# Optimization experiments

Measured on AMD Instinct MI355X. Metric: run time of the kernel, lower is better.

The kernel has to match this reference:

```python
import jax, jax.numpy as jnp
import numpy as np

B, S, D_IN = 4, 2048, 1024
N_HEAD, D_ATTN, D_OUT = 16, 64, 1024
D_H = N_HEAD * D_ATTN  # 1024; NOTE: no head split in original module


def setup_inputs() -> dict:
    key = jax.random.key(0)
    ks = jax.random.split(key, 12)
    s = 1.0 / np.sqrt(D_IN)
    inp = {
        "q": jax.random.normal(ks[0], (B, S, D_IN), dtype=jnp.float32),
        "k": jax.random.normal(ks[1], (B, S, D_IN), dtype=jnp.float32),
        "v": jax.random.normal(ks[2], (B, S, D_IN), dtype=jnp.float32),
        "mask": jax.random.randint(ks[3], (B, S, S), 0, 2, dtype=jnp.int32),
        "Wq": jax.random.normal(ks[4], (D_H, D_IN), dtype=jnp.float32) * s,
        "bq": jnp.zeros((D_H,), dtype=jnp.float32),
        "Wk": jax.random.normal(ks[5], (D_H, D_IN), dtype=jnp.float32) * s,
        "bk": jnp.zeros((D_H,), dtype=jnp.float32),
        "Wv": jax.random.normal(ks[6], (D_H, D_IN), dtype=jnp.float32) * s,
        "bv": jnp.zeros((D_H,), dtype=jnp.float32),
        "Wo": jax.random.normal(ks[7], (D_OUT, D_H), dtype=jnp.float32) * (1.0 / np.sqrt(D_H)),
        "bo": jnp.zeros((D_OUT,), dtype=jnp.float32),
    }
    return inp


def reference(q, k, v, mask, Wq, bq, Wk, bk, Wv, bv, Wo, bo):
    # manual QKV projections (torch Linear: x @ W.T + b)
    Q = q @ Wq.T + bq  # [B,S,D_H]
    K = k @ Wk.T + bk
    V = v @ Wv.T + bv
    d_k = Q.shape[-1]  # full concatenated dim (no head split, faithful)
    e = jnp.einsum("bsd,btd->bst", Q, K) / jnp.sqrt(jnp.float32(d_k))  # [B,S,S]
    MASK_FILL = jnp.float32(-(2 ** 15))  # original uses -2**15 regardless of dtype
    e = jnp.where(mask == 0, MASK_FILL, e)
    a = jax.nn.softmax(e, axis=-1)
    y = jnp.einsum("bst,btd->bsd", a, V)  # [B,S,D_H]
    return y @ Wo.T + bo  # [B,S,D_OUT]
```

## Files before the change

### kernel.cpp

```cpp
#include <hip/hip_runtime.h>
#include <hip/hip_bf16.h>

#define B_   4
#define S_   2048
#define DIN  1024
#define DH   1024
#define DOUT 1024

typedef __attribute__((ext_vector_type(8))) __bf16 bf16x8;
typedef __attribute__((ext_vector_type(4))) float floatx4;
typedef unsigned short u16;
typedef unsigned int u32;

__device__ inline u16 f2bf(float f) {
  union { float f; u32 u; } x; x.f = f;
  u32 r = x.u + 0x7fffu + ((x.u >> 16) & 1u);
  return (u16)(r >> 16);
}

__global__ __launch_bounds__(256)
void cast_f32_bf16(const float* __restrict__ in, u16* __restrict__ out, long n4) {
  long i = (long)blockIdx.x * 256 + threadIdx.x;
  if (i >= n4) return;
  float4 v = ((const float4*)in)[i];
  ushort4 o;
  o.x = f2bf(v.x); o.y = f2bf(v.y); o.z = f2bf(v.z); o.w = f2bf(v.w);
  ((ushort4*)out)[i] = o;
}

__global__ __launch_bounds__(256)
void gather_bias(const float* __restrict__ b0, const float* __restrict__ b1,
                 const float* __restrict__ b2, float* __restrict__ dst) {
  int i = blockIdx.x * 256 + threadIdx.x;
  if (i < DH) dst[i] = b0[i];
  else if (i < 2 * DH) dst[i] = b1[i - DH];
  else if (i < 3 * DH) dst[i] = b2[i - 2 * DH];
}

__global__ __launch_bounds__(256)
void transpose_bf16(const u16* __restrict__ in, u16* __restrict__ out) {
  __shared__ u16 t[32][33];
  const int b = blockIdx.z;
  const int r0 = blockIdx.y * 32, c0 = blockIdx.x * 32;
  const int tx = threadIdx.x & 31, ty = threadIdx.x >> 5;
  const u16* ib = in + (long)b * S_ * DH;
  u16* ob = out + (long)b * DH * S_;
#pragma unroll
  for (int i = 0; i < 4; ++i) {
    int r = ty + i * 8;
    t[r][tx] = ib[(long)(r0 + r) * DH + (c0 + tx)];
  }
  __syncthreads();
#pragma unroll
  for (int i = 0; i < 4; ++i) {
    int r = ty + i * 8;
    ob[(long)(c0 + r) * S_ + (r0 + tx)] = t[tx][r];
  }
}

__global__ __launch_bounds__(256)
void softmax_row(const u16* __restrict__ E, u16* __restrict__ A) {
  const long row = blockIdx.x;
  const _Float16* e = (const _Float16*)(E + row * (long)S_);
  u16* a = A + row * (long)S_;
  const int tid = threadIdx.x;
  const int w = tid >> 6, l = tid & 63;
  __shared__ float sred[8];

  typedef __attribute__((ext_vector_type(8))) _Float16 f16x8;
  f16x8 ev = *(const f16x8*)(e + tid * 8);
  float p[8];
#pragma unroll
  for (int j = 0; j < 8; ++j) p[j] = (float)ev[j];

  float mx = p[0];
#pragma unroll
  for (int j = 1; j < 8; ++j) mx = fmaxf(mx, p[j]);
#pragma unroll
  for (int o = 32; o > 0; o >>= 1) mx = fmaxf(mx, __shfl_xor(mx, o));
  if (l == 0) sred[w] = mx;
  __syncthreads();
  mx = fmaxf(fmaxf(sred[0], sred[1]), fmaxf(sred[2], sred[3]));

  float sum = 0.f;
#pragma unroll
  for (int j = 0; j < 8; ++j) { p[j] = __expf(p[j] - mx); sum += p[j]; }
#pragma unroll
  for (int o = 32; o > 0; o >>= 1) sum += __shfl_xor(sum, o);
  if (l == 0) sred[4 + w] = sum;
  __syncthreads();
  sum = sred[4] + sred[5] + sred[6] + sred[7];
  const float inv = 1.0f / sum;

  ushort4 o0, o1;
  o0.x = f2bf(p[0] * inv); o0.y = f2bf(p[1] * inv);
  o0.z = f2bf(p[2] * inv); o0.w = f2bf(p[3] * inv);
  o1.x = f2bf(p[4] * inv); o1.y = f2bf(p[5] * inv);
  o1.z = f2bf(p[6] * inv); o1.w = f2bf(p[7] * inv);
  ((ushort4*)a)[tid * 2]     = o0;
  ((ushort4*)a)[tid * 2 + 1] = o1;
}

#define EPI_BF16_BIAS 0
#define EPI_F16_MASK  1
#define EPI_BF16      2
#define EPI_F32_BIAS  3

#define BARRIER() do { asm volatile("" ::: "memory"); __builtin_amdgcn_s_barrier(); \
                       asm volatile("" ::: "memory"); } while (0)
#define WAITVM(N) asm volatile("s_waitcnt vmcnt(" #N ")" ::: "memory")

template <int EPI, int BN>
__global__ __launch_bounds__(512, 2)
void gemm256(const u16* __restrict__ A, const u16* __restrict__ Bm,
             void* __restrict__ C, const float* __restrict__ bias,
             const int* __restrict__ mask,
             int M, int N, int K, float scale,
             long sA, long sB, long sC, long sMask, long sBias,
             int nbx, int nby) {
  constexpr int NBR = BN / 128;
  constexpr int BUFSTRIDE = (2 + NBR) * 8192;
  constexpr int MFR = (BN == 256) ? 8 : 4;
  constexpr int MH  = MFR / 2;
  __shared__ u16 lds_[2 * BUFSTRIDE];

  const int tid = threadIdx.x;
  const int w  = tid >> 6;
  const int l  = tid & 63;
  const int wr = (BN == 256) ? (w >> 2) : (w >> 1);
  const int wc = (BN == 256) ? (w & 3) : (w & 1);
  const int lr = l & 15;
  const int q  = l >> 4;
  const int wrowb = wr * (MFR * 16);

  const int flat = blockIdx.x;
  const int cpx = (nbx * nby * gridDim.x / (nbx * nby)) >> 3;
  const int swz = (flat & 7) * (gridDim.x >> 3) + (flat >> 3);
  (void)cpx;
  const int bx = swz % nbx;
  const int rest = swz / nbx;
  const int by = rest % nby;
  const int bz = rest / nby;

  const long arow0 = (long)by * 256;
  const long bcol0 = (long)bx * BN;
  const u16* Ab = A + bz * sA + arow0 * K;
  const u16* Bb = Bm + bz * sB + bcol0 * K;

  const int nt = K >> 6;

  const int st_row = tid >> 3;
  const int st_ks  = (tid & 7) ^ (st_row & 7);

#define STAGE(GB, MATB, H, TT) do {                                           \
    const int _b = (TT) & 1;                                                  \
    const long _k0 = (long)(TT) * 64;                                         \
    _Pragma("unroll")                                                         \
    for (int _j = 0; _j < 2; ++_j) {                                          \
      const u16* _src = (GB) + (long)((H) * 128 + _j * 64 + st_row) * K       \
                        + _k0 + st_ks * 8;                                    \
      u16* _dst = &lds_[_b * BUFSTRIDE + ((MATB) + (H)) * 8192                \
                        + _j * 4096 + tid * 8];                               \
      __builtin_amdgcn_global_load_lds(                                       \
          (const __attribute__((address_space(1))) u32*)_src,                 \
          (__attribute__((address_space(3))) u32*)_dst, 16, 0, 0);            \
    }                                                                         \
  } while (0)

  floatx4 acc[MFR][4] = {};
  bf16x8 a[MH][2];
  bf16x8 b[2][2][2];

#define LDSOFF(BUF, MATB, _r, _s) \
    ((BUF) * BUFSTRIDE + ((MATB) + ((_r) >> 7)) * 8192 + ((_r) & 127) * 64 \
     + (((_s) ^ ((_r) & 7)) * 8))

#define LOAD_A(MHI, BUF) do {                                                 \
    _Pragma("unroll")                                                         \
    for (int _m = 0; _m < MH; ++_m)                                           \
      _Pragma("unroll")                                                       \
      for (int _kk = 0; _kk < 2; ++_kk) {                                     \
        const int _r = wrowb + (MHI) * (MH * 16) + _m * 16 + lr;              \
        const int _s = _kk * 4 + q;                                           \
        a[_m][_kk] = *(const bf16x8*)&lds_[LDSOFF(BUF, 0, _r, _s)];           \
      }                                                                       \
  } while (0)

#define LOAD_B(NHI, BUF) do {                                                 \
    _Pragma("unroll")                                                         \
    for (int _n = 0; _n < 2; ++_n)                                            \
      _Pragma("unroll")                                                       \
      for (int _kk = 0; _kk < 2; ++_kk) {                                     \
        const int _c = wc * 64 + (NHI) * 32 + _n * 16 + lr;                   \
        const int _s = _kk * 4 + q;                                           \
        b[NHI][_n][_kk] = *(const bf16x8*)&lds_[LDSOFF(BUF, 2, _c, _s)];      \
      }                                                                       \
  } while (0)

#define DO_Q(MHI, NHI) do {                                                   \
    __builtin_amdgcn_s_setprio(1);                                            \
    _Pragma("unroll")                                                         \
    for (int _m = 0; _m < MH; ++_m)                                           \
      _Pragma("unroll")                                                       \
      for (int _n = 0; _n < 2; ++_n)                                          \
        _Pragma("unroll")                                                     \
        for (int _kk = 0; _kk < 2; ++_kk)                                     \
          acc[(MHI)*MH + _m][(NHI)*2 + _n] = __builtin_amdgcn_mfma_f32_16x16x32_bf16( \
              a[_m][_kk], b[NHI][_n][_kk], acc[(MHI)*MH + _m][(NHI)*2 + _n], 0, 0, 0); \
    __builtin_amdgcn_s_setprio(0);                                            \
  } while (0)

  STAGE(Ab, 0, 0, 0); STAGE(Ab, 0, 1, 0);
  STAGE(Bb, 2, 0, 0); if constexpr (BN == 256) STAGE(Bb, 2, 1, 0);
  if (nt > 1) {
    STAGE(Bb, 2, 0, 1); if constexpr (BN == 256) STAGE(Bb, 2, 1, 1);
    if constexpr (BN == 256) { WAITVM(4); } else { WAITVM(2); }
  } else {
    WAITVM(0);
  }
  BARRIER();

  for (int t = 0; t < nt; ++t) {
    const int bmain = t & 1;
    LOAD_A(0, bmain); LOAD_B(0, bmain);
    if (t + 1 < nt) STAGE(Ab, 0, 0, t + 1);
    BARRIER();
    DO_Q(0, 0);
    BARRIER();
    LOAD_B(1, bmain);
    if (t + 1 < nt) STAGE(Ab, 0, 1, t + 1);
    BARRIER();
    DO_Q(0, 1);
    BARRIER();
    LOAD_A(1, bmain);
    if (t + 2 < nt) STAGE(Bb, 2, 0, t + 2);
    BARRIER();
    DO_Q(1, 1);
    BARRIER();
    if constexpr (BN == 256) { if (t + 2 < nt) STAGE(Bb, 2, 1, t + 2); }
    DO_Q(1, 0);
    if (t + 2 < nt) {
      if constexpr (BN == 256) { WAITVM(4); } else { WAITVM(2); }
    } else {
      WAITVM(0);
    }
    BARRIER();
  }

#undef STAGE
#undef LOAD_A
#undef LOAD_B
#undef DO_Q
#undef LDSOFF

  const int r4 = q * 4;
#pragma unroll
  for (int mf = 0; mf < MFR; ++mf)
#pragma unroll
    for (int nf = 0; nf < 4; ++nf)
#pragma unroll
      for (int r = 0; r < 4; ++r) {
        const long row = arow0 + wrowb + mf * 16 + r4 + r;
        const long col = bcol0 + wc * 64 + nf * 16 + lr;
        float v = acc[mf][nf][r];
        if constexpr (EPI == EPI_BF16_BIAS) {
          v += bias[bz * sBias + col];
          ((u16*)C)[bz * sC + row * N + col] = f2bf(v);
        } else if constexpr (EPI == EPI_BF16) {
          ((u16*)C)[bz * sC + row * N + col] = f2bf(v);
        } else if constexpr (EPI == EPI_F32_BIAS) {
          v += bias[bz * sBias + col];
          ((float*)C)[bz * sC + row * N + col] = v;
        } else {
          v *= scale;
          const int mk = mask[bz * sMask + row * (long)N + col];
          _Float16 hv = (_Float16)((mk == 0) ? -32768.0f : v);
          ((_Float16*)C)[bz * sC + row * N + col] = hv;
        }
      }
}

extern "C" void kernel_launch(void* const* d_in, const int* in_sizes, int n_in,
                              void* d_out, int out_size, void* d_ws, size_t ws_size,
                              hipStream_t stream) {
  const float* q    = (const float*)d_in[0];
  const float* k    = (const float*)d_in[1];
  const float* v    = (const float*)d_in[2];
  const int*   mask = (const int*)d_in[3];
  const float* Wq   = (const float*)d_in[4];
  const float* bq   = (const float*)d_in[5];
  const float* Wk   = (const float*)d_in[6];
  const float* bk   = (const float*)d_in[7];
  const float* Wv   = (const float*)d_in[8];
  const float* bv   = (const float*)d_in[9];
  const float* Wo   = (const float*)d_in[10];
  const float* bo   = (const float*)d_in[11];

  const long BS = (long)B_ * S_;
  const long nQ = BS * DH;
  const long nW = (long)DH * DIN;
  const long nE = (long)B_ * S_ * S_;

  char* ws = (char*)d_ws;
  size_t off = 0;
  auto alloc = [&](size_t bytes) {
    void* p = ws + off; off += (bytes + 255) & ~(size_t)255; return p;
  };

  u16* qb   = (u16*)alloc(nQ * 2);
  u16* kb   = (u16*)alloc(nQ * 2);
  u16* vb   = (u16*)alloc(nQ * 2);
  u16* wqb  = (u16*)alloc(nW * 2);
  u16* wkb  = (u16*)alloc(nW * 2);
  u16* wvb  = (u16*)alloc(nW * 2);
  u16* wob  = (u16*)alloc(nW * 2);
  u16* Qb   = (u16*)alloc(nQ * 2);
  u16* Kb   = (u16*)alloc(nQ * 2);
  u16* Vb   = (u16*)alloc(nQ * 2);
  u16* VT   = (u16*)alloc(nQ * 2);
  u16* E    = (u16*)alloc(nE * 2);
  float* bcat = (float*)alloc(3 * DH * 4);
  u16* Apb = qb;
  u16* Yb  = vb;

  auto cast = [&](const float* src, u16* dst, long n) {
    long n4 = n / 4;
    cast_f32_bf16<<<dim3((unsigned)((n4 + 255) / 256)), 256, 0, stream>>>(src, dst, n4);
  };
  cast(q, qb, nQ); cast(k, kb, nQ); cast(v, vb, nQ);
  cast(Wq, wqb, nW); cast(Wk, wkb, nW); cast(Wv, wvb, nW); cast(Wo, wob, nW);
  gather_bias<<<dim3(12), 256, 0, stream>>>(bq, bk, bv, bcat);

  gemm256<EPI_BF16_BIAS, 128><<<dim3(768), 512, 0, stream>>>(qb, wqb, Qb, bcat, nullptr,
      (int)BS, DH, DIN, 1.f, nQ, nW, nQ, 0, DH, DH / 128, (int)(BS / 256));

  {
    dim3 g(DH / 32, S_ / 32, B_);
    transpose_bf16<<<g, 256, 0, stream>>>(Vb, VT);
  }

  gemm256<EPI_F16_MASK, 256><<<dim3(256), 512, 0, stream>>>(Qb, Kb, (void*)E, nullptr, mask,
      S_, S_, DH, 0.03125f,
      (long)S_ * DH, (long)S_ * DH, (long)S_ * S_, (long)S_ * S_, 0,
      S_ / 256, S_ / 256);

  softmax_row<<<dim3((unsigned)(B_ * S_)), 256, 0, stream>>>(E, Apb);

  gemm256<EPI_BF16, 128><<<dim3(256), 512, 0, stream>>>(Apb, VT, Yb, nullptr, nullptr,
      S_, DH, S_, 1.f,
      (long)S_ * S_, (long)DH * S_, (long)S_ * DH, 0, 0,
      DH / 128, S_ / 256);

  gemm256<EPI_F32_BIAS, 128><<<dim3(256), 512, 0, stream>>>(Yb, wob, d_out, bo, nullptr,
      (int)BS, DOUT, DH, 1.f, 0, 0, 0, 0, 0,
      DOUT / 128, (int)(BS / 256));
}
```

Baseline: 247.9 us.

## Fuse softmax exp into QK GEMM epilogue and defer normalization to PV

```diff
diff --git a/kernel.cpp b/kernel.cpp
--- a/kernel.cpp
+++ b/kernel.cpp
@@ -18,14 +18,31 @@
   return (u16)(r >> 16);
 }
 
+#define BARRIER() do { asm volatile("" ::: "memory"); __builtin_amdgcn_s_barrier(); \
+                       asm volatile("" ::: "memory"); } while (0)
+#define WAITVM(N) asm volatile("s_waitcnt vmcnt(" #N ")" ::: "memory")
+
 __global__ __launch_bounds__(256)
-void cast_f32_bf16(const float* __restrict__ in, u16* __restrict__ out, long n4) {
-  long i = (long)blockIdx.x * 256 + threadIdx.x;
-  if (i >= n4) return;
-  float4 v = ((const float4*)in)[i];
+void cast_all(const float* __restrict__ q, const float* __restrict__ k,
+              const float* __restrict__ v, const float* __restrict__ w0,
+              const float* __restrict__ w1, const float* __restrict__ w2,
+              const float* __restrict__ w3, u16* __restrict__ dst) {
+  const long nQ = (long)B_ * S_ * DIN;
+  const long nW = (long)DH * DIN;
+  long b = blockIdx.x;
+  const float* src; long doff;
+  if (b < 8192)       { src = q;  doff = 0;            }
+  else if (b < 16384) { src = k;  doff = nQ;     b -= 8192;  }
+  else if (b < 24576) { src = v;  doff = 2 * nQ; b -= 16384; }
+  else if (b < 25600) { src = w0; doff = 3 * nQ; b -= 24576; }
+  else if (b < 26624) { src = w1; doff = 3 * nQ + nW;     b -= 25600; }
+  else if (b < 27648) { src = w2; doff = 3 * nQ + 2 * nW; b -= 26624; }
+  else                { src = w3; doff = 3 * nQ + 3 * nW; b -= 27648; }
+  long i = b * 256 + threadIdx.x;
+  float4 vv = ((const float4*)src)[i];
   ushort4 o;
-  o.x = f2bf(v.x); o.y = f2bf(v.y); o.z = f2bf(v.z); o.w = f2bf(v.w);
-  ((ushort4*)out)[i] = o;
+  o.x = f2bf(vv.x); o.y = f2bf(vv.y); o.z = f2bf(vv.z); o.w = f2bf(vv.w);
+  ((ushort4*)(dst + doff))[i] = o;
 }
 
 __global__ __launch_bounds__(256)
@@ -59,100 +76,47 @@
 }
 
 __global__ __launch_bounds__(256)
-void softmax_row(const u16* __restrict__ E, u16* __restrict__ A) {
-  const long row = blockIdx.x;
-  const _Float16* e = (const _Float16*)(E + row * (long)S_);
-  u16* a = A + row * (long)S_;
-  const int tid = threadIdx.x;
-  const int w = tid >> 6, l = tid & 63;
-  __shared__ float sred[8];
-
-  typedef __attribute__((ext_vector_type(8))) _Float16 f16x8;
-  f16x8 ev = *(const f16x8*)(e + tid * 8);
-  float p[8];
-#pragma unroll
-  for (int j = 0; j < 8; ++j) p[j] = (float)ev[j];
-
-  float mx = p[0];
-#pragma unroll
-  for (int j = 1; j < 8; ++j) mx = fmaxf(mx, p[j]);
-#pragma unroll
-  for (int o = 32; o > 0; o >>= 1) mx = fmaxf(mx, __shfl_xor(mx, o));
-  if (l == 0) sred[w] = mx;
-  __syncthreads();
-  mx = fmaxf(fmaxf(sred[0], sred[1]), fmaxf(sred[2], sred[3]));
-
-  float sum = 0.f;
-#pragma unroll
-  for (int j = 0; j < 8; ++j) { p[j] = __expf(p[j] - mx); sum += p[j]; }
-#pragma unroll
-  for (int o = 32; o > 0; o >>= 1) sum += __shfl_xor(sum, o);
-  if (l == 0) sred[4 + w] = sum;
-  __syncthreads();
-  sum = sred[4] + sred[5] + sred[6] + sred[7];
-  const float inv = 1.0f / sum;
-
-  ushort4 o0, o1;
-  o0.x = f2bf(p[0] * inv); o0.y = f2bf(p[1] * inv);
-  o0.z = f2bf(p[2] * inv); o0.w = f2bf(p[3] * inv);
-  o1.x = f2bf(p[4] * inv); o1.y = f2bf(p[5] * inv);
-  o1.z = f2bf(p[6] * inv); o1.w = f2bf(p[7] * inv);
-  ((ushort4*)a)[tid * 2]     = o0;
-  ((ushort4*)a)[tid * 2 + 1] = o1;
-}
-
-#define EPI_BF16_BIAS 0
-#define EPI_F16_MASK  1
-#define EPI_BF16      2
-#define EPI_F32_BIAS  3
-
-#define BARRIER() do { asm volatile("" ::: "memory"); __builtin_amdgcn_s_barrier(); \
-                       asm volatile("" ::: "memory"); } while (0)
-#define WAITVM(N) asm volatile("s_waitcnt vmcnt(" #N ")" ::: "memory")
-
-template <int EPI, int BN>
+void sumrows(const float* __restrict__ Psum, float* __restrict__ invs) {
+  int i = blockIdx.x * 256 + threadIdx.x;
+  const float4* p = (const float4*)(Psum + (long)i * 8);
+  float4 a = p[0], b = p[1];
+  float s = a.x + a.y + a.z + a.w + b.x + b.y + b.z + b.w;
+  invs[i] = 1.0f / s;
+}
+
 __global__ __launch_bounds__(512, 2)
-void gemm256(const u16* __restrict__ A, const u16* __restrict__ Bm,
-             void* __restrict__ C, const float* __restrict__ bias,
-             const int* __restrict__ mask,
-             int M, int N, int K, float scale,
-             long sA, long sB, long sC, long sMask, long sBias,
-             int nbx, int nby) {
-  constexpr int NBR = BN / 128;
-  constexpr int BUFSTRIDE = (2 + NBR) * 8192;
-  constexpr int MFR = (BN == 256) ? 8 : 4;
-  constexpr int MH  = MFR / 2;
+void gemm_pexp(const u16* __restrict__ Q, const u16* __restrict__ Kb_,
+               u16* __restrict__ P, const int* __restrict__ mask,
+               float* __restrict__ Psum) {
+  constexpr int BUFSTRIDE = 4 * 8192;
   __shared__ u16 lds_[2 * BUFSTRIDE];
 
   const int tid = threadIdx.x;
   const int w  = tid >> 6;
   const int l  = tid & 63;
-  const int wr = (BN == 256) ? (w >> 2) : (w >> 1);
-  const int wc = (BN == 256) ? (w & 3) : (w & 1);
+  const int wr = w >> 2;
+  const int wc = w & 3;
   const int lr = l & 15;
   const int q  = l >> 4;
-  const int wrowb = wr * (MFR * 16);
+  const int wrowb = wr * 128;
 
   const int flat = blockIdx.x;
-  const int cpx = (nbx * nby * gridDim.x / (nbx * nby)) >> 3;
-  const int swz = (flat & 7) * (gridDim.x >> 3) + (flat >> 3);
-  (void)cpx;
-  const int bx = swz % nbx;
-  const int rest = swz / nbx;
-  const int by = rest % nby;
-  const int bz = rest / nby;
+  const int swz = (flat & 7) * ((int)gridDim.x >> 3) + (flat >> 3);
+  const int bx = swz & 7;
+  const int by = (swz >> 3) & 7;
+  const int bz = swz >> 6;
 
   const long arow0 = (long)by * 256;
-  const long bcol0 = (long)bx * BN;
-  const u16* Ab = A + bz * sA + arow0 * K;
-  const u16* Bb = Bm + bz * sB + bcol0 * K;
-
+  const long bcol0 = (long)bx * 256;
+  const int K = DH;
+  const u16* Ab = Q + (long)bz * S_ * DH + arow0 * K;
+  const u16* Bb = Kb_ + (long)bz * S_ * DH + bcol0 * K;
   const int nt = K >> 6;
 
   const int st_row = tid >> 3;
   const int st_ks  = (tid & 7) ^ (st_row & 7);
 
-#define STAGE(GB, MATB, H, TT) do {                                           \
+#define PSTAGE(GB, MATB, H, TT) do {                                          \
     const int _b = (TT) & 1;                                                  \
     const long _k0 = (long)(TT) * 64;                                         \
     _Pragma("unroll")                                                         \
@@ -167,95 +131,260 @@
     }                                                                         \
   } while (0)
 
-  floatx4 acc[MFR][4] = {};
-  bf16x8 a[MH][2];
+  floatx4 acc[8][4] = {};
+  bf16x8 a[4][2];
   bf16x8 b[2][2][2];
 
-#define LDSOFF(BUF, MATB, _r, _s) \
+#define PLDSOFF(BUF, MATB, _r, _s) \
     ((BUF) * BUFSTRIDE + ((MATB) + ((_r) >> 7)) * 8192 + ((_r) & 127) * 64 \
      + (((_s) ^ ((_r) & 7)) * 8))
 
-#define LOAD_A(MHI, BUF) do {                                                 \
-    _Pragma("unroll")                                                         \
-    for (int _m = 0; _m < MH; ++_m)                                           \
+#define PLOAD_A(MHI, BUF) do {                                                \
+    _Pragma("unroll")                                                         \
+    for (int _m = 0; _m < 4; ++_m)                                            \
       _Pragma("unroll")                                                       \
       for (int _kk = 0; _kk < 2; ++_kk) {                                     \
-        const int _r = wrowb + (MHI) * (MH * 16) + _m * 16 + lr;              \
+        const int _r = wrowb + (MHI) * 64 + _m * 16 + lr;                     \
         const int _s = _kk * 4 + q;                                           \
-        a[_m][_kk] = *(const bf16x8*)&lds_[LDSOFF(BUF, 0, _r, _s)];           \
+        a[_m][_kk] = *(const bf16x8*)&lds_[PLDSOFF(BUF, 0, _r, _s)];          \
       }                                                                       \
   } while (0)
 
-#define LOAD_B(NHI, BUF) do {                                                 \
+#define PLOAD_B(NHI, BUF) do {                                                \
     _Pragma("unroll")                                                         \
     for (int _n = 0; _n < 2; ++_n)                                            \
       _Pragma("unroll")                                                       \
       for (int _kk = 0; _kk < 2; ++_kk) {                                     \
         const int _c = wc * 64 + (NHI) * 32 + _n * 16 + lr;                   \
         const int _s = _kk * 4 + q;                                           \
-        b[NHI][_n][_kk] = *(const bf16x8*)&lds_[LDSOFF(BUF, 2, _c, _s)];      \
+        b[NHI][_n][_kk] = *(const bf16x8*)&lds_[PLDSOFF(BUF, 2, _c, _s)];     \
       }                                                                       \
   } while (0)
 
-#define DO_Q(MHI, NHI) do {                                                   \
+#define PDO_Q(MHI, NHI) do {                                                  \
     __builtin_amdgcn_s_setprio(1);                                            \
     _Pragma("unroll")                                                         \
-    for (int _m = 0; _m < MH; ++_m)                                           \
+    for (int _m = 0; _m < 4; ++_m)                                            \
       _Pragma("unroll")                                                       \
       for (int _n = 0; _n < 2; ++_n)                                          \
         _Pragma("unroll")                                                     \
         for (int _kk = 0; _kk < 2; ++_kk)                                     \
-          acc[(MHI)*MH + _m][(NHI)*2 + _n] = __builtin_amdgcn_mfma_f32_16x16x32_bf16( \
-              a[_m][_kk], b[NHI][_n][_kk], acc[(MHI)*MH + _m][(NHI)*2 + _n], 0, 0, 0); \
+          acc[(MHI)*4 + _m][(NHI)*2 + _n] = __builtin_amdgcn_mfma_f32_16x16x32_bf16( \
+              a[_m][_kk], b[NHI][_n][_kk], acc[(MHI)*4 + _m][(NHI)*2 + _n], 0, 0, 0); \
     __builtin_amdgcn_s_setprio(0);                                            \
   } while (0)
 
-  STAGE(Ab, 0, 0, 0); STAGE(Ab, 0, 1, 0);
-  STAGE(Bb, 2, 0, 0); if constexpr (BN == 256) STAGE(Bb, 2, 1, 0);
-  if (nt > 1) {
-    STAGE(Bb, 2, 0, 1); if constexpr (BN == 256) STAGE(Bb, 2, 1, 1);
-    if constexpr (BN == 256) { WAITVM(4); } else { WAITVM(2); }
-  } else {
-    WAITVM(0);
-  }
+  PSTAGE(Ab, 0, 0, 0); PSTAGE(Ab, 0, 1, 0);
+  PSTAGE(Bb, 2, 0, 0); PSTAGE(Bb, 2, 1, 0);
+  PSTAGE(Bb, 2, 0, 1); PSTAGE(Bb, 2, 1, 1);
+  WAITVM(4);
   BARRIER();
 
   for (int t = 0; t < nt; ++t) {
     const int bmain = t & 1;
-    LOAD_A(0, bmain); LOAD_B(0, bmain);
-    if (t + 1 < nt) STAGE(Ab, 0, 0, t + 1);
-    BARRIER();
-    DO_Q(0, 0);
-    BARRIER();
-    LOAD_B(1, bmain);
-    if (t + 1 < nt) STAGE(Ab, 0, 1, t + 1);
-    BARRIER();
-    DO_Q(0, 1);
-    BARRIER();
-    LOAD_A(1, bmain);
-    if (t + 2 < nt) STAGE(Bb, 2, 0, t + 2);
-    BARRIER();
-    DO_Q(1, 1);
-    BARRIER();
-    if constexpr (BN == 256) { if (t + 2 < nt) STAGE(Bb, 2, 1, t + 2); }
-    DO_Q(1, 0);
-    if (t + 2 < nt) {
-      if constexpr (BN == 256) { WAITVM(4); } else { WAITVM(2); }
-    } else {
-      WAITVM(0);
+    PLOAD_A(0, bmain); PLOAD_B(0, bmain);
+    if (t + 1 < nt) PSTAGE(Ab, 0, 0, t + 1);
+    BARRIER();
+    PDO_Q(0, 0);
+    BARRIER();
+    PLOAD_B(1, bmain);
+    if (t + 1 < nt) PSTAGE(Ab, 0, 1, t + 1);
+    BARRIER();
+    PDO_Q(0, 1);
+    BARRIER();
+    PLOAD_A(1, bmain);
+    if (t + 2 < nt) PSTAGE(Bb, 2, 0, t + 2);
+    BARRIER();
+    PDO_Q(1, 1);
+    BARRIER();
+    if (t + 2 < nt) PSTAGE(Bb, 2, 1, t + 2);
+    PDO_Q(1, 0);
+    if (t + 2 < nt) { WAITVM(4); } else { WAITVM(0); }
+    BARRIER();
+  }
+
+#undef PSTAGE
+#undef PLOAD_A
+#undef PLOAD_B
+#undef PDO_Q
+#undef PLDSOFF
+
+  const int r4 = q * 4;
+  float rsum[8][4];
+#pragma unroll
+  for (int mf = 0; mf < 8; ++mf)
+#pragma unroll
+    for (int r = 0; r < 4; ++r) rsum[mf][r] = 0.f;
+
+#pragma unroll
+  for (int mf = 0; mf < 8; ++mf)
+#pragma unroll
+    for (int nf = 0; nf < 4; ++nf)
+#pragma unroll
+      for (int r = 0; r < 4; ++r) {
+        const long row = arow0 + wrowb + mf * 16 + r4 + r;
+        const long col = bcol0 + wc * 64 + nf * 16 + lr;
+        const int mk = mask[(long)bz * S_ * S_ + row * S_ + col];
+        float p = 0.f;
+        if (mk != 0) p = __expf(acc[mf][nf][r] * 0.03125f);
+        P[(long)bz * S_ * S_ + row * S_ + col] = f2bf(p);
+        rsum[mf][r] += p;
+      }
+
+  float* sc = (float*)lds_;
+#pragma unroll
+  for (int mf = 0; mf < 8; ++mf)
+#pragma unroll
+    for (int r = 0; r < 4; ++r) {
+      float s = rsum[mf][r];
+      s += __shfl_xor(s, 1); s += __shfl_xor(s, 2);
+      s += __shfl_xor(s, 4); s += __shfl_xor(s, 8);
+      if (lr == 0) sc[(wrowb + mf * 16 + r4 + r) * 4 + wc] = s;
     }
-    BARRIER();
-  }
-
-#undef STAGE
-#undef LOAD_A
-#undef LOAD_B
-#undef DO_Q
-#undef LDSOFF
+  __syncthreads();
+  if (tid < 256) {
+    float tot = sc[tid * 4] + sc[tid * 4 + 1] + sc[tid * 4 + 2] + sc[tid * 4 + 3];
+    Psum[((long)bz * S_ + arow0 + tid) * 8 + bx] = tot;
+  }
+}
+
+#define EPI_BF16_BIAS     0
+#define EPI_BF16_ROWSCALE 1
+#define EPI_F32_BIAS      2
+
+template <int EPI>
+__global__ __launch_bounds__(512, 2)
+void gemm128x2(const u16* __restrict__ A, const u16* __restrict__ Bm,
+               void* __restrict__ C, const float* __restrict__ bias,
+               const float* __restrict__ rowinv,
+               int M, int N, int K,
+               long sA, long sB, long sC, long sBias,
+               int nbx, int nby) {
+  __shared__ u16 lAbuf[2 * 16384];
+  __shared__ u16 lBbuf[3 * 8192];
+
+  const int tid = threadIdx.x;
+  const int w  = tid >> 6;
+  const int l  = tid & 63;
+  const int wr = w >> 1;
+  const int wc = w & 1;
+  const int lr = l & 15;
+  const int q  = l >> 4;
+  const int wrowb = wr * 64;
+
+  const int flat = blockIdx.x;
+  const int swz = (flat & 7) * ((int)gridDim.x >> 3) + (flat >> 3);
+  const int bx = swz % nbx;
+  const int rest = swz / nbx;
+  const int by = rest % nby;
+  const int bz = rest / nby;
+
+  const long arow0 = (long)by * 256;
+  const long bcol0 = (long)bx * 128;
+  const u16* Ab = A + bz * sA + arow0 * K;
+  const u16* Bb = Bm + bz * sB + bcol0 * K;
+  const int nt = K >> 6;
+
+  const int st_row = tid >> 3;
+  const int st_ks  = (tid & 7) ^ (st_row & 7);
+
+#define STAGE_A(H, TT) do {                                                   \
+    const int _ab = (TT) & 1;                                                 \
+    const long _k0 = (long)(TT) * 64;                                         \
+    _Pragma("unroll")                                                         \
+    for (int _j = 0; _j < 2; ++_j) {                                          \
+      const u16* _src = Ab + (long)((H) * 128 + _j * 64 + st_row) * K         \
+                        + _k0 + st_ks * 8;                                    \
+      u16* _dst = &lAbuf[_ab * 16384 + (H) * 8192 + _j * 4096 + tid * 8];     \
+      __builtin_amdgcn_global_load_lds(                                       \
+          (const __attribute__((address_space(1))) u32*)_src,                 \
+          (__attribute__((address_space(3))) u32*)_dst, 16, 0, 0);            \
+    }                                                                         \
+  } while (0)
+
+#define STAGE_B(TT) do {                                                      \
+    const int _bb = (TT) % 3;                                                 \
+    const long _k0 = (long)(TT) * 64;                                         \
+    _Pragma("unroll")                                                         \
+    for (int _j = 0; _j < 2; ++_j) {                                          \
+      const u16* _src = Bb + (long)(_j * 64 + st_row) * K + _k0 + st_ks * 8;  \
+      u16* _dst = &lBbuf[_bb * 8192 + _j * 4096 + tid * 8];                   \
+      __builtin_amdgcn_global_load_lds(                                       \
+          (const __attribute__((address_space(1))) u32*)_src,                 \
+          (__attribute__((address_space(3))) u32*)_dst, 16, 0, 0);            \
+    }                                                                         \
+  } while (0)
+
+  floatx4 acc[4][4] = {};
+  bf16x8 a[4][2];
+  bf16x8 b[2][2];
+
+#define LOAD_A_ALL(BUF) do {                                                  \
+    _Pragma("unroll")                                                         \
+    for (int _m = 0; _m < 4; ++_m)                                            \
+      _Pragma("unroll")                                                       \
+      for (int _kk = 0; _kk < 2; ++_kk) {                                     \
+        const int _r = wrowb + _m * 16 + lr;                                  \
+        const int _s = _kk * 4 + q;                                           \
+        a[_m][_kk] = *(const bf16x8*)&lAbuf[(BUF) * 16384 + (_r >> 7) * 8192  \
+                     + (_r & 127) * 64 + ((_s ^ (_r & 7)) * 8)];              \
+      }                                                                       \
+  } while (0)
+
+#define LOAD_BH(NH, BUF) do {                                                 \
+    _Pragma("unroll")                                                         \
+    for (int _n = 0; _n < 2; ++_n)                                            \
+      _Pragma("unroll")                                                       \
+      for (int _kk = 0; _kk < 2; ++_kk) {                                     \
+        const int _c = wc * 64 + (NH) * 32 + _n * 16 + lr;                    \
+        const int _s = _kk * 4 + q;                                           \
+        b[_n][_kk] = *(const bf16x8*)&lBbuf[(BUF) * 8192 + _c * 64            \
+                     + ((_s ^ (_c & 7)) * 8)];                                \
+      }                                                                       \
+  } while (0)
+
+#define DO_NH(NH) do {                                                        \
+    __builtin_amdgcn_s_setprio(1);                                            \
+    _Pragma("unroll")                                                         \
+    for (int _m = 0; _m < 4; ++_m)                                            \
+      _Pragma("unroll")                                                       \
+      for (int _n = 0; _n < 2; ++_n)                                          \
+        _Pragma("unroll")                                                     \
+        for (int _kk = 0; _kk < 2; ++_kk)                                     \
+          acc[_m][(NH)*2 + _n] = __builtin_amdgcn_mfma_f32_16x16x32_bf16(     \
+              a[_m][_kk], b[_n][_kk], acc[_m][(NH)*2 + _n], 0, 0, 0);         \
+    __builtin_amdgcn_s_setprio(0);                                            \
+  } while (0)
+
+  STAGE_A(0, 0); STAGE_A(1, 0);
+  STAGE_B(0);
+  if (nt > 1) { STAGE_B(1); WAITVM(2); } else { WAITVM(0); }
+  BARRIER();
+
+  for (int t = 0; t < nt; ++t) {
+    const int ab = t & 1, bb = t % 3;
+    LOAD_A_ALL(ab); LOAD_BH(0, bb);
+    if (t + 1 < nt) { STAGE_A(0, t + 1); STAGE_A(1, t + 1); }
+    BARRIER();
+    DO_NH(0);
+    BARRIER();
+    LOAD_BH(1, bb);
+    if (t + 2 < nt) STAGE_B(t + 2);
+    BARRIER();
+    DO_NH(1);
+    if (t + 2 < nt) { WAITVM(2); } else { WAITVM(0); }
+    BARRIER();
+  }
+
+#undef STAGE_A
+#undef STAGE_B
+#undef LOAD_A_ALL
+#undef LOAD_BH
+#undef DO_NH
 
   const int r4 = q * 4;
 #pragma unroll
-  for (int mf = 0; mf < MFR; ++mf)
+  for (int mf = 0; mf < 4; ++mf)
 #pragma unroll
     for (int nf = 0; nf < 4; ++nf)
 #pragma unroll
@@ -266,16 +395,12 @@
         if constexpr (EPI == EPI_BF16_BIAS) {
           v += bias[bz * sBias + col];
           ((u16*)C)[bz * sC + row * N + col] = f2bf(v);
-        } else if constexpr (EPI == EPI_BF16) {
+        } else if constexpr (EPI == EPI_BF16_ROWSCALE) {
+          v *= rowinv[bz * sBias + row];
           ((u16*)C)[bz * sC + row * N + col] = f2bf(v);
-        } else if constexpr (EPI == EPI_F32_BIAS) {
-          v += bias[bz * sBias + col];
+        } else {
+          v += bias[col];
           ((float*)C)[bz * sC + row * N + col] = v;
-        } else {
-          v *= scale;
-          const int mk = mask[bz * sMask + row * (long)N + col];
-          _Float16 hv = (_Float16)((mk == 0) ? -32768.0f : v);
-          ((_Float16*)C)[bz * sC + row * N + col] = hv;
         }
       }
 }
@@ -315,43 +440,34 @@
   u16* wvb  = (u16*)alloc(nW * 2);
   u16* wob  = (u16*)alloc(nW * 2);
   u16* Qb   = (u16*)alloc(nQ * 2);
-  u16* Kb   = (u16*)alloc(nQ * 2);
+  u16* Kbf  = (u16*)alloc(nQ * 2);
   u16* Vb   = (u16*)alloc(nQ * 2);
   u16* VT   = (u16*)alloc(nQ * 2);
-  u16* E    = (u16*)alloc(nE * 2);
+  u16* P    = (u16*)alloc(nE * 2);
+  float* Psum = (float*)alloc(BS * 8 * 4);
+  float* invs = (float*)alloc(BS * 4);
   float* bcat = (float*)alloc(3 * DH * 4);
-  u16* Apb = qb;
   u16* Yb  = vb;
 
-  auto cast = [&](const float* src, u16* dst, long n) {
-    long n4 = n / 4;
-    cast_f32_bf16<<<dim3((unsigned)((n4 + 255) / 256)), 256, 0, stream>>>(src, dst, n4);
-  };
-  cast(q, qb, nQ); cast(k, kb, nQ); cast(v, vb, nQ);
-  cast(Wq, wqb, nW); cast(Wk, wkb, nW); cast(Wv, wvb, nW); cast(Wo, wob, nW);
+  cast_all<<<dim3(28672), 256, 0, stream>>>(q, k, v, Wq, Wk, Wv, Wo, qb);
   gather_bias<<<dim3(12), 256, 0, stream>>>(bq, bk, bv, bcat);
 
-  gemm256<EPI_BF16_BIAS, 128><<<dim3(768), 512, 0, stream>>>(qb, wqb, Qb, bcat, nullptr,
-      (int)BS, DH, DIN, 1.f, nQ, nW, nQ, 0, DH, DH / 128, (int)(BS / 256));
+  gemm128x2<EPI_BF16_BIAS><<<dim3(768), 512, 0, stream>>>(qb, wqb, Qb, bcat,
+      nullptr, (int)BS, DH, DIN, nQ, nW, nQ, DH, 8, 32);
 
   {
     dim3 g(DH / 32, S_ / 32, B_);
     transpose_bf16<<<g, 256, 0, stream>>>(Vb, VT);
   }
 
-  gemm256<EPI_F16_MASK, 256><<<dim3(256), 512, 0, stream>>>(Qb, Kb, (void*)E, nullptr, mask,
-      S_, S_, DH, 0.03125f,
-      (long)S_ * DH, (long)S_ * DH, (long)S_ * S_, (long)S_ * S_, 0,
-      S_ / 256, S_ / 256);
-
-  softmax_row<<<dim3((unsigned)(B_ * S_)), 256, 0, stream>>>(E, Apb);
-
-  gemm256<EPI_BF16, 128><<<dim3(256), 512, 0, stream>>>(Apb, VT, Yb, nullptr, nullptr,
-      S_, DH, S_, 1.f,
-      (long)S_ * S_, (long)DH * S_, (long)S_ * DH, 0, 0,
-      DH / 128, S_ / 256);
-
-  gemm256<EPI_F32_BIAS, 128><<<dim3(256), 512, 0, stream>>>(Yb, wob, d_out, bo, nullptr,
-      (int)BS, DOUT, DH, 1.f, 0, 0, 0, 0, 0,
-      DOUT / 128, (int)(BS / 256));
-}
+  gemm_pexp<<<dim3(256), 512, 0, stream>>>(Qb, Kbf, P, mask, Psum);
+
+  sumrows<<<dim3(32), 256, 0, stream>>>(Psum, invs);
+
+  gemm128x2<EPI_BF16_ROWSCALE><<<dim3(256), 512, 0, stream>>>(P, VT, Yb,
+      nullptr, invs, S_, DH, S_,
+      (long)S_ * S_, (long)DH * S_, (long)S_ * DH, S_, 8, 8);
+
+  gemm128x2<EPI_F32_BIAS><<<dim3(256), 512, 0, stream>>>(Yb, wob, d_out, bo,
+      nullptr, (int)BS, DOUT, DH, 0, 0, 0, 0, 8, 32);
+}
```

New measurement: 229.5 us. 1.08x faster.
